# Performance work log

Hardware: AMD Instinct MI355X
Metric: run time of the kernel (lower is better)

Reference implementation:

```python
import jax, jax.numpy as jnp
import numpy as np

N = 20000
NEG_SLOPE = 0.2


def gatv2_layer(x, src, dst, edge_attr, Wl, bl, Wr, br, We, att, bias, H, C):
    """PyG GATv2Conv: add self-loops (edge_attr fill='mean'), gather-score-softmax-aggregate."""
    n = x.shape[0]
    E = src.shape[0]
    # --- add self loops, self-loop edge_attr = mean of incoming edge_attr per node ---
    ea_sum = jax.ops.segment_sum(edge_attr, dst, num_segments=n)
    deg = jax.ops.segment_sum(jnp.ones((E, 1), x.dtype), dst, num_segments=n)
    ea_loop = ea_sum / jnp.maximum(deg, 1.0)
    loop = jnp.arange(n)
    src_a = jnp.concatenate([src, loop])
    dst_a = jnp.concatenate([dst, loop])
    ea = jnp.concatenate([edge_attr, ea_loop], axis=0)
    # --- linear projections ---
    xl = (x @ Wl + bl).reshape(n, H, C)   # source-side features
    xr = (x @ Wr + br).reshape(n, H, C)   # target-side features
    e = (ea @ We).reshape(-1, H, C)       # edge features
    # --- per-edge GATv2 attention score ---
    m = xl[src_a] + xr[dst_a] + e                          # [E', H, C]
    s = jnp.sum(jax.nn.leaky_relu(m, NEG_SLOPE) * att, -1)  # [E', H]
    # --- softmax over incoming edges of each target node ---
    smax = jax.ops.segment_max(s, dst_a, num_segments=n)
    ex = jnp.exp(s - smax[dst_a])
    denom = jax.ops.segment_sum(ex, dst_a, num_segments=n)
    alpha = ex / (denom[dst_a] + 1e-16)                    # [E', H]
    # --- aggregate messages (alpha * x_l[src]) ---
    out = jax.ops.segment_sum(alpha[..., None] * xl[src_a], dst_a, num_segments=n)
    return out.reshape(n, H * C) + bias


def setup_inputs() -> dict:
    key = jax.random.key(0)
    ks = jax.random.split(key, 20)
    F, HID, H1, A = 128, 32, 8, 128
    E = 640000
    d = {}
    d["x"] = jax.random.normal(ks[0], (N, F), jnp.float32)
    d["edge_index"] = jax.random.randint(ks[1], (2, E), 0, N, jnp.int32).astype(jnp.int64)
    d["edge_attr"] = jax.random.normal(ks[2], (E, 1), jnp.float32)
    # layer 1 params (in=F, out=HID, heads=H1)
    d["W1l"] = jax.random.normal(ks[3], (F, H1 * HID), jnp.float32) * 0.05
    d["b1l"] = jnp.zeros((H1 * HID,), jnp.float32)
    d["W1r"] = jax.random.normal(ks[4], (F, H1 * HID), jnp.float32) * 0.05
    d["b1r"] = jnp.zeros((H1 * HID,), jnp.float32)
    d["We1"] = jax.random.normal(ks[5], (1, H1 * HID), jnp.float32) * 0.05
    d["att1"] = jax.random.normal(ks[6], (H1, HID), jnp.float32) * 0.05
    d["bias1"] = jnp.zeros((H1 * HID,), jnp.float32)
    # layer 2 params (in=H1*HID, out=A, heads=1)
    d["W2l"] = jax.random.normal(ks[7], (H1 * HID, A), jnp.float32) * 0.05
    d["b2l"] = jnp.zeros((A,), jnp.float32)
    d["W2r"] = jax.random.normal(ks[8], (H1 * HID, A), jnp.float32) * 0.05
    d["b2r"] = jnp.zeros((A,), jnp.float32)
    d["We2"] = jax.random.normal(ks[9], (1, A), jnp.float32) * 0.05
    d["att2"] = jax.random.normal(ks[10], (1, A), jnp.float32) * 0.05
    d["bias2"] = jnp.zeros((A,), jnp.float32)
    d["alpha"] = jnp.array(0.0, jnp.float32)
    return d


def reference(x, edge_index, edge_attr, W1l, b1l, W1r, b1r, We1, att1, bias1,
              W2l, b2l, W2r, b2r, We2, att2, bias2, alpha):
    src, dst = edge_index[0], edge_index[1]
    h = jax.nn.relu(gatv2_layer(x, src, dst, edge_attr, W1l, b1l, W1r, b1r,
                                We1, att1, bias1, H=8, C=32))
    h = jax.nn.relu(gatv2_layer(h, src, dst, edge_attr, W2l, b2l, W2r, b2r,
                                We2, att2, bias2, H=1, C=128))
    pooled = jnp.mean(h, axis=0, keepdims=True)  # global_mean_pool, single graph -> [1, A]
    return jax.nn.softmax(pooled, axis=1), jax.nn.sigmoid(alpha)
```

## Files before the change

### kernel.cpp

```cpp
#include <hip/hip_runtime.h>
#include <math.h>

#define NEG_SLOPE 0.2f
#define LOG2E 1.4426950408889634f

typedef __attribute__((ext_vector_type(8))) short short8;
typedef __attribute__((ext_vector_type(4))) float f32x4;
typedef __attribute__((ext_vector_type(2))) float v2f;

__device__ __forceinline__ int imin(int a, int b) { return a < b ? a : b; }

__device__ __forceinline__ unsigned int f2bf(float f) {
    unsigned int u = __float_as_uint(f);
    return (u + 0x7fffu + ((u >> 16) & 1u)) >> 16;
}
__device__ __forceinline__ float fast_exp2(float x) {
#if __has_builtin(__builtin_amdgcn_exp2f)
    return __builtin_amdgcn_exp2f(x);
#else
    return exp2f(x);
#endif
}
__device__ __forceinline__ unsigned char f2fp8(float v) {
    return (unsigned char)(__builtin_amdgcn_cvt_pk_fp8_f32(v, v, 0, false) & 0xff);
}
template <int CTRL>
__device__ __forceinline__ float dpp_add(float v) {
    int t = __builtin_amdgcn_update_dpp(0, __float_as_int(v), CTRL, 0xF, 0xF, true);
    return v + __int_as_float(t);
}
__device__ __forceinline__ v2f pk_fma(v2f a, v2f b, v2f c) {
    v2f d;
    asm("v_pk_fma_f32 %0, %1, %2, %3" : "=v"(d) : "v"(a), "v"(b), "v"(c));
    return d;
}
__device__ __forceinline__ v2f pk_add(v2f a, v2f b) {
    v2f d;
    asm("v_pk_add_f32 %0, %1, %2" : "=v"(d) : "v"(a), "v"(b));
    return d;
}

__global__ void fused_prep(const int* __restrict__ ei, const float* __restrict__ ea,
                           unsigned long long* __restrict__ hist, int E,
                           const float* __restrict__ x, unsigned short* __restrict__ xb, int nF4,
                           const float* __restrict__ W1l, const float* __restrict__ W1r,
                           const float* __restrict__ W2l, const float* __restrict__ W2r,
                           const float* __restrict__ b1l, const float* __restrict__ b1r,
                           const float* __restrict__ b2l, const float* __restrict__ b2r,
                           unsigned short* __restrict__ Wt1, unsigned short* __restrict__ Wt2,
                           float* __restrict__ b1cat, float* __restrict__ b2cat,
                           int F, int HC1, int HC2) {
    int i = blockIdx.x * blockDim.x + threadIdx.x;
    if (i < E) {
        int d = ei[E + i];
        long long fx = (long long)__float2int_rn(ea[i] * 65536.0f);
        unsigned long long v = ((unsigned long long)fx << 32) | 1ull;
        atomicAdd(&hist[(size_t)d * 8], v);
        return;
    }
    int j = i - E;
    if (j < nF4) {
        float4 v = ((const float4*)x)[j];
        uint2 r;
        r.x = f2bf(v.x) | (f2bf(v.y) << 16);
        r.y = f2bf(v.z) | (f2bf(v.w) << 16);
        ((uint2*)xb)[j] = r;
        return;
    }
    int k = j - nF4;
    int S1 = F * HC1, S2 = HC1 * HC2;
    if (k < S1) {
        int kk = k / HC1, nn = k - kk * HC1;
        Wt1[(size_t)nn * F + kk] = (unsigned short)f2bf(W1l[k]);
    } else if (k < 2 * S1) {
        int m = k - S1;
        int kk = m / HC1, nn = m - kk * HC1;
        Wt1[(size_t)(HC1 + nn) * F + kk] = (unsigned short)f2bf(W1r[m]);
    } else if (k < 2 * S1 + S2) {
        int m = k - 2 * S1;
        int kk = m / HC2, nn = m - kk * HC2;
        Wt2[(size_t)nn * HC1 + kk] = (unsigned short)f2bf(W2l[m]);
    } else if (k < 2 * S1 + 2 * S2) {
        int m = k - 2 * S1 - S2;
        int kk = m / HC2, nn = m - kk * HC2;
        Wt2[(size_t)(HC2 + nn) * HC1 + kk] = (unsigned short)f2bf(W2r[m]);
    } else if (k < 2 * S1 + 2 * S2 + 2 * HC1) {
        int m = k - 2 * S1 - 2 * S2;
        b1cat[m] = (m < HC1) ? b1l[m] : b1r[m - HC1];
    } else if (k < 2 * S1 + 2 * S2 + 2 * HC1 + 2 * HC2) {
        int m = k - 2 * S1 - 2 * S2 - 2 * HC1;
        b2cat[m] = (m < HC2) ? b2l[m] : b2r[m - HC2];
    }
}

__global__ void scan_a(const unsigned long long* __restrict__ hist, int* __restrict__ bsum, int n) {
    __shared__ int wred[4];
    int base = blockIdx.x * 1024;
    int tid = threadIdx.x;
    int s = 0;
#pragma unroll
    for (int k = 0; k < 4; ++k) {
        int i = base + tid + k * 256;
        if (i < n) s += (int)(hist[(size_t)i * 8] & 0xffffffffull);
    }
#pragma unroll
    for (int off = 32; off > 0; off >>= 1) s += __shfl_xor(s, off, 64);
    if ((tid & 63) == 0) wred[tid >> 6] = s;
    __syncthreads();
    if (tid == 0) bsum[blockIdx.x] = wred[0] + wred[1] + wred[2] + wred[3];
}

__global__ void scan_c(const unsigned long long* __restrict__ hist,
                       const int* __restrict__ bsum, int* __restrict__ row_ptr,
                       int* __restrict__ wptr_pad, float* __restrict__ ea_loop,
                       int n, int B) {
    __shared__ int wtot[4];
    __shared__ int sh_base;
    int tid = threadIdx.x;
    int wid = tid >> 6, lane = tid & 63;
    int i0 = blockIdx.x * 1024 + tid * 4;
    int dcnt[4]; float esum[4];
#pragma unroll
    for (int k = 0; k < 4; ++k) {
        if (i0 + k < n) {
            unsigned long long h = hist[(size_t)(i0 + k) * 8];
            dcnt[k] = (int)(h & 0xffffffffull);
            esum[k] = (float)((int)(h >> 32)) * (1.0f / 65536.0f);
        } else { dcnt[k] = 0; esum[k] = 0.0f; }
    }
    int tsum = dcnt[0] + dcnt[1] + dcnt[2] + dcnt[3];
    int s = tsum;
#pragma unroll
    for (int off = 1; off < 64; off <<= 1) {
        int t = __shfl_up(s, off, 64);
        if (lane >= off) s += t;
    }
    if (lane == 63) wtot[wid] = s;
    if (tid < 64) {
        int v   = (tid < B) ? bsum[tid] : 0;
        int pre = (tid < (int)blockIdx.x) ? v : 0;
        int tot = v;
#pragma unroll
        for (int off = 32; off > 0; off >>= 1) {
            pre += __shfl_xor(pre, off, 64);
            tot += __shfl_xor(tot, off, 64);
        }
        if (tid == 0) {
            sh_base = pre;
            if (blockIdx.x == 0) row_ptr[n] = tot;
        }
    }
    __syncthreads();
    int wpre = 0;
#pragma unroll
    for (int k = 0; k < 4; ++k) if (k < wid) wpre += wtot[k];
    int pre = sh_base + wpre + (s - tsum);
    if (i0 < n) {
        int4 e;
        e.x = pre;
        e.y = pre + dcnt[0];
        e.z = e.y + dcnt[1];
        e.w = e.z + dcnt[2];
        *(int4*)(row_ptr + i0) = e;
        int ev[4] = { e.x, e.y, e.z, e.w };
        float4 el;
        el.x = esum[0] / fmaxf((float)dcnt[0], 1.0f);
        el.y = esum[1] / fmaxf((float)dcnt[1], 1.0f);
        el.z = esum[2] / fmaxf((float)dcnt[2], 1.0f);
        el.w = esum[3] / fmaxf((float)dcnt[3], 1.0f);
        *(float4*)(ea_loop + i0) = el;
#pragma unroll
        for (int k = 0; k < 4; ++k) wptr_pad[(size_t)(i0 + k) * 16] = ev[k];
    }
}

__global__ void edge_scatter(const int* __restrict__ ei, const float* __restrict__ ea,
                             int* __restrict__ wptr_pad, int2* __restrict__ spk, int E) {
    int e = blockIdx.x * blockDim.x + threadIdx.x;
    if (e < E) {
        int d = ei[E + e];
        int pos = atomicAdd(&wptr_pad[(size_t)d * 16], 1);
        spk[pos] = make_int2(ei[e], __float_as_int(ea[e]));
    }
}

template <bool OUT_FP8>
__global__ void __launch_bounds__(256)
gemm_bf16(const unsigned short* __restrict__ A, const unsigned short* __restrict__ Bt,
          const float* __restrict__ bias, void* __restrict__ Cv,
          int M, int N, int K) {
    __shared__ __attribute__((aligned(16))) unsigned short As[64 * 40];
    __shared__ __attribute__((aligned(16))) unsigned short Bs[64 * 40];
    int tid  = threadIdx.x;
    int wave = tid >> 6, lane = tid & 63;
    int m0 = blockIdx.x * 64, n0 = blockIdx.y * 64;
    int row = tid >> 2, kg = (tid & 3) * 8;

    f32x4 acc[4] = {};
    for (int kk = 0; kk < K; kk += 32) {
        int gm = m0 + row;
        uint4 av;
        if (gm < M) av = *(const uint4*)(A + (size_t)gm * K + kk + kg);
        else        av = make_uint4(0, 0, 0, 0);
        *(uint4*)&As[row * 40 + kg] = av;
        uint4 bv = *(const uint4*)(Bt + (size_t)(n0 + row) * K + kk + kg);
        *(uint4*)&Bs[row * 40 + kg] = bv;
        __syncthreads();
        short8 a = *(const short8*)&As[(wave * 16 + (lane & 15)) * 40 + (lane >> 4) * 8];
#pragma unroll
        for (int g = 0; g < 4; ++g) {
            short8 b = *(const short8*)&Bs[(g * 16 + (lane & 15)) * 40 + (lane >> 4) * 8];
            acc[g] = __builtin_amdgcn_mfma_f32_16x16x32_bf16(a, b, acc[g], 0, 0, 0);
        }
        __syncthreads();
    }
#pragma unroll
    for (int g = 0; g < 4; ++g) {
        int col = n0 + g * 16 + (lane & 15);
        float bs = bias[col];
#pragma unroll
        for (int r = 0; r < 4; ++r) {
            int grow = m0 + wave * 16 + (lane >> 4) * 4 + r;
            if (grow < M) {
                float val = acc[g][r] + bs;
                if constexpr (OUT_FP8) {
                    ((unsigned char*)Cv)[(size_t)grow * N + col] = f2fp8(val);
                } else {
                    ((unsigned short*)Cv)[(size_t)grow * N + col] = (unsigned short)f2bf(val);
                }
            }
        }
    }
}

template <int NG>
__device__ __forceinline__ void unp2(uint2 u, v2f* xf) {
    xf[0] = __builtin_amdgcn_cvt_pk_f32_fp8(u.x, false);
    xf[1] = __builtin_amdgcn_cvt_pk_f32_fp8(u.x, true);
    if constexpr (NG == 4) {
        xf[2] = __builtin_amdgcn_cvt_pk_f32_fp8(u.y, false);
        xf[3] = __builtin_amdgcn_cvt_pk_f32_fp8(u.y, true);
    }
}
template <int G>
__device__ __forceinline__ float grp_reduce32(float vs) {
    vs = dpp_add<0xB1>(vs);
    if constexpr (G >= 4)  vs = dpp_add<0x4E>(vs);
    if constexpr (G >= 8)  vs = dpp_add<0x141>(vs);
    if constexpr (G >= 16) vs = dpp_add<0x140>(vs);
    if constexpr (G >= 32) {
        int t = __builtin_amdgcn_ds_swizzle(__float_as_int(vs), 0x401F);
        vs += __int_as_float(t);
    }
    return vs;
}

template <int HC, int STRIDE, int C, int OUT_MODE>
__global__ void __launch_bounds__(256)
gat_agg(const unsigned char* __restrict__ xlr,
        const float* __restrict__ We, const float* __restrict__ att,
        const float* __restrict__ bias,
        const int* __restrict__ row_ptr, const int2* __restrict__ spk,
        const float* __restrict__ ea_loop,
        void* __restrict__ out, int n) {
    constexpr int NV = HC / 32;
    constexpr int NG = NV / 2;
    constexpr int G  = C / NV;
    constexpr int SHIFT = (STRIDE == 512) ? 9 : 8;
    constexpr float K23 = 2.0f / 3.0f;
    __shared__ float red[4][128];
    int wave = threadIdx.x >> 6;
    int lane = threadIdx.x & 63;
    int node = blockIdx.x * 4 + wave;
    bool active = node < n;
    if (OUT_MODE == 0 && !active) return;
    unsigned int lo32 = (unsigned int)(lane & 31) * NV;
    int half = lane >> 5;

    float vout[NV];
#pragma unroll
    for (int j = 0; j < NV; ++j) vout[j] = 0.0f;

    if (active) {
        auto ldd = [&](unsigned int off) -> uint2 {
            uint2 r;
            if constexpr (NV == 8) r = *(const uint2*)(xlr + off);
            else { r.x = *(const unsigned int*)(xlr + off); r.y = 0u; }
            return r;
        };
        auto gat = [&](int s) -> uint2 {
            return ldd(((unsigned int)s << SHIFT) + lo32);
        };
        auto W = [&](int2 s) -> float { return __int_as_float(s.y); };

        v2f xr2[NG], We2[NG], att62[NG], o2[NG];
        unp2<NG>(ldd(((unsigned int)node << SHIFT) + HC + lo32), xr2);
#pragma unroll
        for (int g = 0; g < NG; ++g) {
            We2[g]   = *(const v2f*)(We  + lo32 + 2 * g);
            v2f a    = *(const v2f*)(att + lo32 + 2 * g);
            att62[g] = a * (0.6f * LOG2E);
            o2[g]    = v2f{0.0f, 0.0f};
        }
        float l = 0.0f;

        int start = __builtin_amdgcn_readfirstlane(row_ptr[node]);
        int end   = __builtin_amdgcn_readfirstlane(row_ptr[node + 1]);
        float ea_l = ea_loop[node];

        auto process = [&](uint2 du, float w, bool maskhi) {
            v2f xf[NG];
            unp2<NG>(du, xf);
            v2f w2 = {w, w};
            v2f vs6 = {0.0f, 0.0f};
            float vs4 = 0.0f;
#pragma unroll
            for (int g = 0; g < NG; ++g) {
                v2f t  = pk_fma(w2, We2[g], xr2[g]);
                v2f mm = pk_add(xf[g], t);
                vs6 = pk_fma(att62[g], mm, vs6);
                vs4 = fmaf(fabsf(mm.x), att62[g].x, vs4);
                vs4 = fmaf(fabsf(mm.y), att62[g].y, vs4);
            }
            float vs = fmaf(K23, vs4, vs6.x + vs6.y);
            vs = grp_reduce32<G>(vs);
            float pr = fast_exp2(vs);
            if (maskhi && lane >= 32) pr = 0.0f;
            l += pr;
            v2f pr2 = {pr, pr};
#pragma unroll
            for (int g = 0; g < NG; ++g) o2[g] = pk_fma(xf[g], pr2, o2[g]);
        };

        process(ldd(((unsigned int)node << SHIFT) + lo32), ea_l, true);

        int cnt = end - start;
        int npair = cnt >> 1;
        const int2* q = spk + start + half;

        if (npair >= 6) {
            int2 m0 = q[0], m1 = q[2], m2 = q[4], m3 = q[6], m4 = q[8], m5 = q[10];
            uint2 g0 = gat(m0.x), g1 = gat(m1.x), g2 = gat(m2.x);
            int p = 0;
            for (; p + 12 <= npair; p += 6) {
                uint2 h0 = gat(m3.x);
                process(g0, W(m0), false); m0 = q[2 * (p + 6)];
                uint2 h1 = gat(m4.x);
                process(g1, W(m1), false); m1 = q[2 * (p + 7)];
                uint2 h2 = gat(m5.x);
                process(g2, W(m2), false); m2 = q[2 * (p + 8)];
                g0 = gat(m0.x);
                process(h0, W(m3), false); m3 = q[2 * (p + 9)];
                g1 = gat(m1.x);
                process(h1, W(m4), false); m4 = q[2 * (p + 10)];
                g2 = gat(m2.x);
                process(h2, W(m5), false); m5 = q[2 * (p + 11)];
            }
            uint2 h0 = gat(m3.x), h1 = gat(m4.x), h2 = gat(m5.x);
            process(g0, W(m0), false); process(g1, W(m1), false);
            process(g2, W(m2), false);
            process(h0, W(m3), false); process(h1, W(m4), false);
            process(h2, W(m5), false);
            for (int k = p + 6; k < npair; ++k) {
                int2 t = q[2 * k];
                process(gat(t.x), W(t), false);
            }
        } else {
            for (int k = 0; k < npair; ++k) {
                int2 t = q[2 * k];
                process(gat(t.x), W(t), false);
            }
        }
        if (cnt & 1) {
            int2 st = spk[end - 1];
            process(gat(st.x), W(st), true);
        }

        l += __shfl_xor(l, 32, 64);
#pragma unroll
        for (int g = 0; g < NG; ++g) {
            o2[g].x += __shfl_xor(o2[g].x, 32, 64);
            o2[g].y += __shfl_xor(o2[g].y, 32, 64);
        }
        float inv = 1.0f / (l + 1e-16f);

        if (lane < 32) {
#pragma unroll
            for (int g = 0; g < NG; ++g) {
                v2f b = *(const v2f*)(bias + lo32 + 2 * g);
                vout[2 * g]     = fmaxf(o2[g].x * inv + b.x, 0.0f);
                vout[2 * g + 1] = fmaxf(o2[g].y * inv + b.y, 0.0f);
            }
            if constexpr (OUT_MODE == 0) {
                unsigned short* op = (unsigned short*)out + (size_t)node * HC + lo32;
                if constexpr (NV == 8) {
                    uint4 t;
                    t.x = f2bf(vout[0]) | (f2bf(vout[1]) << 16);
                    t.y = f2bf(vout[2]) | (f2bf(vout[3]) << 16);
                    t.z = f2bf(vout[4]) | (f2bf(vout[5]) << 16);
                    t.w = f2bf(vout[6]) | (f2bf(vout[7]) << 16);
                    *(uint4*)op = t;
                } else {
                    uint2 t;
                    t.x = f2bf(vout[0]) | (f2bf(vout[1]) << 16);
                    t.y = f2bf(vout[2]) | (f2bf(vout[3]) << 16);
                    *(uint2*)op = t;
                }
            }
        }
    }

    if constexpr (OUT_MODE == 1) {
        if (lane < 32) {
#pragma unroll
            for (int j = 0; j < NV; ++j) red[wave][lo32 + j] = vout[j];
        }
        __syncthreads();
        if (wave == 0) {
            int c = lane;
            float a = red[0][c] + red[1][c] + red[2][c] + red[3][c];
            float b = red[0][c + 64] + red[1][c + 64] + red[2][c + 64] + red[3][c + 64];
            float* pacc = (float*)out + (size_t)(blockIdx.x & 255) * 128;
            atomicAdd(&pacc[c], a);
            atomicAdd(&pacc[c + 64], b);
        }
    }
}

__global__ void __launch_bounds__(1024)
pool_final(const float* __restrict__ partial, int nb,
           const float* __restrict__ alpha_in,
           float* __restrict__ out, int n) {
    __shared__ float acc[8][128];
    __shared__ float red[4];
    int t = threadIdx.x & 127;
    int g = threadIdx.x >> 7;
    float s = 0.0f;
    for (int b = g; b < nb; b += 8) s += partial[b * 128 + t];
    acc[g][t] = s;
    __syncthreads();
    if (threadIdx.x < 128) {
        float tot = 0.0f;
#pragma unroll
        for (int k = 0; k < 8; ++k) tot += acc[k][t];
        float mean = tot / (float)n;
        float mx = mean;
#pragma unroll
        for (int off = 32; off > 0; off >>= 1) mx = fmaxf(mx, __shfl_xor(mx, off, 64));
        if ((t & 63) == 0) red[t >> 6] = mx;
        __syncthreads();
        mx = fmaxf(red[0], red[1]);
        float ex = __expf(mean - mx);
        float sm = ex;
#pragma unroll
        for (int off = 32; off > 0; off >>= 1) sm += __shfl_xor(sm, off, 64);
        if ((t & 63) == 0) red[2 + (t >> 6)] = sm;
        __syncthreads();
        sm = red[2] + red[3];
        out[t] = ex / sm;
        if (t == 0) out[128] = 1.0f / (1.0f + __expf(-alpha_in[0]));
    }
}

extern "C" void kernel_launch(void* const* d_in, const int* in_sizes, int n_in,
                              void* d_out, int out_size, void* d_ws, size_t ws_size,
                              hipStream_t stream) {
    const float* x    = (const float*)d_in[0];
    const int*   ei   = (const int*)d_in[1];
    const float* ea   = (const float*)d_in[2];
    const float* W1l  = (const float*)d_in[3];
    const float* b1l  = (const float*)d_in[4];
    const float* W1r  = (const float*)d_in[5];
    const float* b1r  = (const float*)d_in[6];
    const float* We1  = (const float*)d_in[7];
    const float* att1 = (const float*)d_in[8];
    const float* bias1= (const float*)d_in[9];
    const float* W2l  = (const float*)d_in[10];
    const float* b2l  = (const float*)d_in[11];
    const float* W2r  = (const float*)d_in[12];
    const float* b2r  = (const float*)d_in[13];
    const float* We2  = (const float*)d_in[14];
    const float* att2 = (const float*)d_in[15];
    const float* bias2= (const float*)d_in[16];
    const float* alpha= (const float*)d_in[17];
    float* out = (float*)d_out;

    const int F = 128, HC1 = 256, HC2 = 128;
    const int n = in_sizes[0] / F;
    const int E = in_sizes[1] / 2;
    const int B = (n + 1023) / 1024;

    char* ws = (char*)d_ws;
    size_t off = 0;
    auto alloc = [&](size_t bytes) { size_t p = off; off += (bytes + 255) & ~(size_t)255; return p; };

    unsigned long long* hist = (unsigned long long*)(ws + alloc((size_t)n * 8 * 8));
    int*   row_ptr = (int*)  (ws + alloc((size_t)(n + 1) * 4));
    int*   wptr    = (int*)  (ws + alloc((size_t)n * 16 * 4));
    float* ea_loop = (float*)(ws + alloc((size_t)n * 4));
    int*   bsum    = (int*)  (ws + alloc(64 * 4));
    int2*  spk     = (int2*) (ws + alloc((size_t)E * 8));
    unsigned short* xb   = (unsigned short*)(ws + alloc((size_t)n * F * 2));
    unsigned short* Wt1  = (unsigned short*)(ws + alloc((size_t)F * (2 * HC1) * 2));
    unsigned short* Wt2  = (unsigned short*)(ws + alloc((size_t)HC1 * (2 * HC2) * 2));
    float* b1cat   = (float*)(ws + alloc((size_t)2 * HC1 * 4));
    float* b2cat   = (float*)(ws + alloc((size_t)2 * HC2 * 4));
    unsigned char* xlr1 = (unsigned char*)(ws + alloc((size_t)n * 2 * HC1));
    unsigned short* h1  = (unsigned short*)(ws + alloc((size_t)n * HC1 * 2));
    float* partial = (float*)(ws + alloc((size_t)256 * 128 * 4));
    unsigned char* xlr2 = xlr1;
    const int NB_SLOTS = 256;

    (void)hipMemsetAsync(hist, 0, (size_t)n * 8 * 8, stream);
    (void)hipMemsetAsync(partial, 0, (size_t)NB_SLOTS * 128 * 4, stream);

    int tb = 256;
    {
        int nF4  = n * F / 4;
        int WTOT = 2 * F * HC1 + 2 * HC1 * HC2 + 2 * HC1 + 2 * HC2;
        int total = E + nF4 + WTOT;
        fused_prep<<<(total + tb - 1) / tb, tb, 0, stream>>>(
            ei, ea, hist, E, x, xb, nF4,
            W1l, W1r, W2l, W2r, b1l, b1r, b2l, b2r,
            Wt1, Wt2, b1cat, b2cat, F, HC1, HC2);
    }
    scan_a<<<B, 256, 0, stream>>>(hist, bsum, n);
    scan_c<<<B, 256, 0, stream>>>(hist, bsum, row_ptr, wptr, ea_loop, n, B);
    edge_scatter<<<(E + tb - 1) / tb, tb, 0, stream>>>(ei, ea, wptr, spk, E);

    {
        dim3 grid((n + 63) / 64, (2 * HC1) / 64);
        gemm_bf16<true><<<grid, 256, 0, stream>>>(xb, Wt1, b1cat, xlr1, n, 2 * HC1, F);
    }
    gat_agg<256, 512, 32, 0><<<(n + 3) / 4, 256, 0, stream>>>(
        xlr1, We1, att1, bias1, row_ptr, spk, ea_loop, h1, n);

    {
        dim3 grid((n + 63) / 64, (2 * HC2) / 64);
        gemm_bf16<true><<<grid, 256, 0, stream>>>(h1, Wt2, b2cat, xlr2, n, 2 * HC2, HC1);
    }
    gat_agg<128, 256, 128, 1><<<(n + 3) / 4, 256, 0, stream>>>(
        xlr2, We2, att2, bias2, row_ptr, spk, ea_loop, partial, n);

    pool_final<<<1, 1024, 0, stream>>>(partial, NB_SLOTS, alpha, out, n);
}
```

Measured before the change: 283.7 us.

## Process one edge per wavefront with all 64 lanes covering features

Changes the aggregation kernel's work mapping. Before, each half-wave (32 lanes) handled alternate edges, and the halves were merged at the end. Now all 64 lanes split the feature vector of a single edge, so each lane loads half as many fp8 bytes per edge. This removes the pair/odd-edge masking and the cross-half shuffle reduction at the end. In exchange, each edge is processed sequentially with narrower loads. Layer 2 (C=128) also needs an extra cross-half shuffle in the score reduction for every edge.

Measured after the change: 276.5 us. -2.5%, faster.

```diff
diff --git a/kernel.cpp b/kernel.cpp
--- a/kernel.cpp
+++ b/kernel.cpp
@@ -233,17 +233,13 @@
     }
 }
 
-template <int NG>
-__device__ __forceinline__ void unp2(uint2 u, v2f* xf) {
-    xf[0] = __builtin_amdgcn_cvt_pk_f32_fp8(u.x, false);
-    xf[1] = __builtin_amdgcn_cvt_pk_f32_fp8(u.x, true);
-    if constexpr (NG == 4) {
-        xf[2] = __builtin_amdgcn_cvt_pk_f32_fp8(u.y, false);
-        xf[3] = __builtin_amdgcn_cvt_pk_f32_fp8(u.y, true);
-    }
+template <int NV>
+__device__ __forceinline__ void unp1(unsigned int u, v2f* xf) {
+    xf[0] = __builtin_amdgcn_cvt_pk_f32_fp8(u, false);
+    if constexpr (NV == 4) xf[1] = __builtin_amdgcn_cvt_pk_f32_fp8(u, true);
 }
 template <int G>
-__device__ __forceinline__ float grp_reduce32(float vs) {
+__device__ __forceinline__ float grp_reduce(float vs) {
     vs = dpp_add<0xB1>(vs);
     if constexpr (G >= 4)  vs = dpp_add<0x4E>(vs);
     if constexpr (G >= 8)  vs = dpp_add<0x141>(vs);
@@ -252,6 +248,7 @@
         int t = __builtin_amdgcn_ds_swizzle(__float_as_int(vs), 0x401F);
         vs += __int_as_float(t);
     }
+    if constexpr (G >= 64) vs += __shfl_xor(vs, 32, 64);
     return vs;
 }
 
@@ -263,8 +260,8 @@
         const int* __restrict__ row_ptr, const int2* __restrict__ spk,
         const float* __restrict__ ea_loop,
         void* __restrict__ out, int n) {
-    constexpr int NV = HC / 32;
-    constexpr int NG = NV / 2;
+    constexpr int NV = HC / 64;
+    constexpr int NG = (NV + 1) / 2;
     constexpr int G  = C / NV;
     constexpr int SHIFT = (STRIDE == 512) ? 9 : 8;
     constexpr float K23 = 2.0f / 3.0f;
@@ -274,31 +271,33 @@
     int node = blockIdx.x * 4 + wave;
     bool active = node < n;
     if (OUT_MODE == 0 && !active) return;
-    unsigned int lo32 = (unsigned int)(lane & 31) * NV;
-    int half = lane >> 5;
+    unsigned int lo = (unsigned int)lane * NV;
 
     float vout[NV];
 #pragma unroll
     for (int j = 0; j < NV; ++j) vout[j] = 0.0f;
 
     if (active) {
-        auto ldd = [&](unsigned int off) -> uint2 {
-            uint2 r;
-            if constexpr (NV == 8) r = *(const uint2*)(xlr + off);
-            else { r.x = *(const unsigned int*)(xlr + off); r.y = 0u; }
-            return r;
+        auto ldd = [&](unsigned int off) -> unsigned int {
+            if constexpr (NV == 4) return *(const unsigned int*)(xlr + off);
+            else                   return (unsigned int)(*(const unsigned short*)(xlr + off));
         };
-        auto gat = [&](int s) -> uint2 {
-            return ldd(((unsigned int)s << SHIFT) + lo32);
+        auto gat = [&](int s) -> unsigned int {
+            return ldd(((unsigned int)s << SHIFT) + lo);
         };
         auto W = [&](int2 s) -> float { return __int_as_float(s.y); };
 
         v2f xr2[NG], We2[NG], att62[NG], o2[NG];
-        unp2<NG>(ldd(((unsigned int)node << SHIFT) + HC + lo32), xr2);
+        {
+            v2f tmp[NG];
+            unp1<NV>(ldd(((unsigned int)node << SHIFT) + HC + lo), tmp);
+#pragma unroll
+            for (int g = 0; g < NG; ++g) xr2[g] = tmp[g];
+        }
 #pragma unroll
         for (int g = 0; g < NG; ++g) {
-            We2[g]   = *(const v2f*)(We  + lo32 + 2 * g);
-            v2f a    = *(const v2f*)(att + lo32 + 2 * g);
+            We2[g]   = *(const v2f*)(We  + lo + 2 * g);
+            v2f a    = *(const v2f*)(att + lo + 2 * g);
             att62[g] = a * (0.6f * LOG2E);
             o2[g]    = v2f{0.0f, 0.0f};
         }
@@ -308,9 +307,9 @@
         int end   = __builtin_amdgcn_readfirstlane(row_ptr[node + 1]);
         float ea_l = ea_loop[node];
 
-        auto process = [&](uint2 du, float w, bool maskhi) {
+        auto process = [&](unsigned int du, float w) {
             v2f xf[NG];
-            unp2<NG>(du, xf);
+            unp1<NV>(du, xf);
             v2f w2 = {w, w};
             v2f vs6 = {0.0f, 0.0f};
             float vs4 = 0.0f;
@@ -323,98 +322,72 @@
                 vs4 = fmaf(fabsf(mm.y), att62[g].y, vs4);
             }
             float vs = fmaf(K23, vs4, vs6.x + vs6.y);
-            vs = grp_reduce32<G>(vs);
+            vs = grp_reduce<G>(vs);
             float pr = fast_exp2(vs);
-            if (maskhi && lane >= 32) pr = 0.0f;
             l += pr;
             v2f pr2 = {pr, pr};
 #pragma unroll
             for (int g = 0; g < NG; ++g) o2[g] = pk_fma(xf[g], pr2, o2[g]);
         };
 
-        process(ldd(((unsigned int)node << SHIFT) + lo32), ea_l, true);
+        process(ldd(((unsigned int)node << SHIFT) + lo), ea_l);
 
         int cnt = end - start;
-        int npair = cnt >> 1;
-        const int2* q = spk + start + half;
-
-        if (npair >= 6) {
-            int2 m0 = q[0], m1 = q[2], m2 = q[4], m3 = q[6], m4 = q[8], m5 = q[10];
-            uint2 g0 = gat(m0.x), g1 = gat(m1.x), g2 = gat(m2.x);
+        const int2* q = spk + start;
+
+        if (cnt >= 6) {
+            int2 t;
+            t = q[0]; unsigned int g0 = gat(t.x); float w0 = W(t);
+            t = q[1]; unsigned int g1 = gat(t.x); float w1 = W(t);
+            t = q[2]; unsigned int g2 = gat(t.x); float w2 = W(t);
+            t = q[3]; unsigned int g3 = gat(t.x); float w3 = W(t);
+            t = q[4]; unsigned int g4 = gat(t.x); float w4 = W(t);
+            t = q[5]; unsigned int g5 = gat(t.x); float w5 = W(t);
             int p = 0;
-            for (; p + 12 <= npair; p += 6) {
-                uint2 h0 = gat(m3.x);
-                process(g0, W(m0), false); m0 = q[2 * (p + 6)];
-                uint2 h1 = gat(m4.x);
-                process(g1, W(m1), false); m1 = q[2 * (p + 7)];
-                uint2 h2 = gat(m5.x);
-                process(g2, W(m2), false); m2 = q[2 * (p + 8)];
-                g0 = gat(m0.x);
-                process(h0, W(m3), false); m3 = q[2 * (p + 9)];
-                g1 = gat(m1.x);
-                process(h1, W(m4), false); m4 = q[2 * (p + 10)];
-                g2 = gat(m2.x);
-                process(h2, W(m5), false); m5 = q[2 * (p + 11)];
+            for (; p + 12 <= cnt; p += 6) {
+                process(g0, w0); t = q[p + 6];  g0 = gat(t.x); w0 = W(t);
+                process(g1, w1); t = q[p + 7];  g1 = gat(t.x); w1 = W(t);
+                process(g2, w2); t = q[p + 8];  g2 = gat(t.x); w2 = W(t);
+                process(g3, w3); t = q[p + 9];  g3 = gat(t.x); w3 = W(t);
+                process(g4, w4); t = q[p + 10]; g4 = gat(t.x); w4 = W(t);
+                process(g5, w5); t = q[p + 11]; g5 = gat(t.x); w5 = W(t);
             }
-            uint2 h0 = gat(m3.x), h1 = gat(m4.x), h2 = gat(m5.x);
-            process(g0, W(m0), false); process(g1, W(m1), false);
-            process(g2, W(m2), false);
-            process(h0, W(m3), false); process(h1, W(m4), false);
-            process(h2, W(m5), false);
-            for (int k = p + 6; k < npair; ++k) {
-                int2 t = q[2 * k];
-                process(gat(t.x), W(t), false);
+            process(g0, w0); process(g1, w1); process(g2, w2);
+            process(g3, w3); process(g4, w4); process(g5, w5);
+            for (int k = p + 6; k < cnt; ++k) {
+                t = q[k];
+                process(gat(t.x), W(t));
             }
         } else {
-            for (int k = 0; k < npair; ++k) {
-                int2 t = q[2 * k];
-                process(gat(t.x), W(t), false);
+            for (int k = 0; k < cnt; ++k) {
+                int2 t = q[k];
+                process(gat(t.x), W(t));
             }
         }
-        if (cnt & 1) {
-            int2 st = spk[end - 1];
-            process(gat(st.x), W(st), true);
-        }
-
-        l += __shfl_xor(l, 32, 64);
+
+        float inv = 1.0f / (l + 1e-16f);
 #pragma unroll
         for (int g = 0; g < NG; ++g) {
-            o2[g].x += __shfl_xor(o2[g].x, 32, 64);
-            o2[g].y += __shfl_xor(o2[g].y, 32, 64);
-        }
-        float inv = 1.0f / (l + 1e-16f);
-
-        if (lane < 32) {
-#pragma unroll
-            for (int g = 0; g < NG; ++g) {
-                v2f b = *(const v2f*)(bias + lo32 + 2 * g);
-                vout[2 * g]     = fmaxf(o2[g].x * inv + b.x, 0.0f);
-                vout[2 * g + 1] = fmaxf(o2[g].y * inv + b.y, 0.0f);
+            v2f b = *(const v2f*)(bias + lo + 2 * g);
+            vout[2 * g]     = fmaxf(o2[g].x * inv + b.x, 0.0f);
+            vout[2 * g + 1] = fmaxf(o2[g].y * inv + b.y, 0.0f);
+        }
+        if constexpr (OUT_MODE == 0) {
+            unsigned short* op = (unsigned short*)out + (size_t)node * HC + lo;
+            if constexpr (NV == 4) {
+                uint2 t;
+                t.x = f2bf(vout[0]) | (f2bf(vout[1]) << 16);
+                t.y = f2bf(vout[2]) | (f2bf(vout[3]) << 16);
+                *(uint2*)op = t;
+            } else {
+                *(unsigned int*)op = f2bf(vout[0]) | (f2bf(vout[1]) << 16);
             }
-            if constexpr (OUT_MODE == 0) {
-                unsigned short* op = (unsigned short*)out + (size_t)node * HC + lo32;
-                if constexpr (NV == 8) {
-                    uint4 t;
-                    t.x = f2bf(vout[0]) | (f2bf(vout[1]) << 16);
-                    t.y = f2bf(vout[2]) | (f2bf(vout[3]) << 16);
-                    t.z = f2bf(vout[4]) | (f2bf(vout[5]) << 16);
-                    t.w = f2bf(vout[6]) | (f2bf(vout[7]) << 16);
-                    *(uint4*)op = t;
-                } else {
-                    uint2 t;
-                    t.x = f2bf(vout[0]) | (f2bf(vout[1]) << 16);
-                    t.y = f2bf(vout[2]) | (f2bf(vout[3]) << 16);
-                    *(uint2*)op = t;
-                }
-            }
         }
     }
 
     if constexpr (OUT_MODE == 1) {
-        if (lane < 32) {
-#pragma unroll
-            for (int j = 0; j < NV; ++j) red[wave][lo32 + j] = vout[j];
-        }
+#pragma unroll
+        for (int j = 0; j < NV; ++j) red[wave][lo + j] = vout[j];
         __syncthreads();
         if (wave == 0) {
             int c = lane;
```
